# Optimization experiments

Measured on AMD Instinct MI355X. Metric: run time of the kernel, lower is better.

## Reference

```python
import jax, jax.numpy as jnp
import numpy as np

VOCAB = 100000
EMBED = 64
SENT = 20
MEM = 50
BATCH = 32
HOPS = 3
PAD_ID = 0


def position_encoding(sentence_size, embedding_size):
    # Section 4.1 of MemN2N paper, vectorized. Returns [sentence_size, embedding_size].
    i = np.arange(1, embedding_size + 1, dtype=np.float32)[:, None]   # [E,1]
    j = np.arange(1, sentence_size + 1, dtype=np.float32)[None, :]    # [1,S]
    enc = (i - (embedding_size + 1) / 2.0) * (j - (sentence_size + 1) / 2.0)
    enc = 1.0 + 4.0 * enc / embedding_size / sentence_size
    enc[:, -1] = 1.0
    return jnp.asarray(enc.T, dtype=jnp.float32)  # [S,E]


def setup_inputs() -> dict:
    key = jax.random.key(0)
    k1, k2, k3, k4 = jax.random.split(key, 4)
    stories = jax.random.randint(k1, (BATCH, MEM, SENT), 0, VOCAB, dtype=jnp.int64 if jax.config.jax_enable_x64 else jnp.int32)
    queries = jax.random.randint(k2, (BATCH, SENT), 0, VOCAB, dtype=jnp.int64 if jax.config.jax_enable_x64 else jnp.int32)
    A = jax.random.normal(k3, (VOCAB, EMBED), dtype=jnp.float32) * 0.1
    C = jax.random.normal(k4, (HOPS, VOCAB, EMBED), dtype=jnp.float32) * 0.1
    # padding_idx=PAD_ID rows are zero, as in nn.Embedding(padding_idx=...)
    A = A.at[PAD_ID].set(0.0)
    C = C.at[:, PAD_ID].set(0.0)
    encoding = position_encoding(SENT, EMBED)
    return {"stories": stories, "queries": queries, "A": A, "C": C, "encoding": encoding}


def reference(stories, queries, A, C, encoding):
    # queries: [B,S], stories: [B,M,S], A: [V,E], C: [hops,V,E], encoding: [S,E]
    q_emb = A[queries]                                # [B,S,E]
    u = (q_emb * encoding).sum(axis=1)                # [B,E]
    for hop in range(HOPS):
        table_in = A if hop == 0 else C[hop - 1]
        emb_A = table_in[stories]                     # [B,M,S,E]
        m = (emb_A * encoding).sum(axis=2)            # [B,M,E]
        dotted = jnp.einsum('bme,be->bm', m, u)       # [B,M]
        probs = jax.nn.softmax(dotted, axis=-1)       # [B,M]
        emb_C = C[hop][stories]                       # [B,M,S,E]
        c = (emb_C * encoding).sum(axis=2)            # [B,M,E]
        o = jnp.einsum('bm,bme->be', probs, c)        # [B,E]
        u = u + o
    return u @ C[-1].T                                # [B,V]
```

## Files before the change

kernel.cpp:

```cpp
#include <hip/hip_runtime.h>
#include <hip/hip_bf16.h>

#define VOCAB 100000
#define EMBED 64
#define SENT  20
#define MEM   50
#define BATCH 32
#define HOPS  3

#define NSET  4
#define NSLOT (NSET * BATCH * MEM)
#define NVT   (VOCAB / 16)

typedef __attribute__((ext_vector_type(8))) short short8v;
typedef __attribute__((ext_vector_type(4))) float f32x4;

__device__ __forceinline__ float bfr(unsigned short x) {
    union { unsigned int u; float f; } cv;
    cv.u = ((unsigned int)x) << 16;
    return cv.f;
}

__device__ __forceinline__ bool is_bf16(const void* enc) {
    return ((const unsigned int*)enc)[639] == 0x3F803F80u;
}

template<bool BF>
__device__ __forceinline__ float ldT(const void* p, size_t idx) {
    if constexpr (BF) return bfr(((const unsigned short*)p)[idx]);
    else              return ((const float*)p)[idx];
}

__device__ __forceinline__ float wave_sum(float d) {
#pragma unroll
    for (int off = 32; off > 0; off >>= 1) d += __shfl_xor(d, off, 64);
    return d;
}

template<bool BF>
__device__ __forceinline__ void gather_body(const int* __restrict__ stories,
                                            const int* __restrict__ queries,
                                            const void* __restrict__ A,
                                            const void* __restrict__ C,
                                            const void* __restrict__ enc,
                                            float* __restrict__ mc_ws,
                                            float* __restrict__ u0g)
{
    const int tid = threadIdx.x;
    const int e   = tid & 63;
    const int gw  = blockIdx.x * 4 + (tid >> 6);
    const size_t VE = (size_t)VOCAB * EMBED;

    float encr[SENT];
#pragma unroll
    for (int s = 0; s < SENT; ++s) encr[s] = ldT<BF>(enc, s * EMBED + e);

    if (gw < NSLOT) {
        const int t  = gw / (BATCH * MEM);
        const int bm = gw % (BATCH * MEM);
        const void* T   = (t == 0) ? A : C;
        const size_t to = (t == 0) ? 0 : (size_t)(t - 1) * VE;

        int wst = (e < SENT) ? stories[bm * SENT + e] : 0;
        float acc = 0.f;
#pragma unroll
        for (int s = 0; s < SENT; ++s) {
            int w = __shfl(wst, s, 64);
            acc += ldT<BF>(T, to + (size_t)w * EMBED + e) * encr[s];
        }
        mc_ws[gw * EMBED + e] = acc;
    } else if (gw < NSLOT + BATCH) {
        const int b = gw - NSLOT;
        int wq = (e < SENT) ? queries[b * SENT + e] : 0;
        float u = 0.f;
#pragma unroll
        for (int s = 0; s < SENT; ++s) {
            int w = __shfl(wq, s, 64);
            u += ldT<BF>(A, (size_t)w * EMBED + e) * encr[s];
        }
        u0g[b * EMBED + e] = u;
    }
}

__global__ __launch_bounds__(256) void k_gather(
    const int* __restrict__ stories,
    const int* __restrict__ queries,
    const void* __restrict__ A,
    const void* __restrict__ C,
    const void* __restrict__ enc,
    float* __restrict__ mc_ws,
    float* __restrict__ u0g)
{
    if (is_bf16(enc)) gather_body<true >(stories, queries, A, C, enc, mc_ws, u0g);
    else              gather_body<false>(stories, queries, A, C, enc, mc_ws, u0g);
}

__global__ __launch_bounds__(256) void k_recur2(
    const float* __restrict__ mc_ws,
    const float* __restrict__ u0g,
    float* __restrict__ u3g,
    unsigned short* __restrict__ u3bf)
{
    const int b    = blockIdx.x;
    const int tid  = threadIdx.x;
    const int lane = tid & 63;
    const int widx = tid >> 6;

    __shared__ float mc[NSET][MEM][65];
    __shared__ float uls[EMBED];
    __shared__ float ols[4][EMBED];

    for (int idx = tid; idx < NSET * MEM * 16; idx += 256) {
        int t  = idx / (MEM * 16);
        int r  = idx % (MEM * 16);
        int mm = r >> 4;
        int e4 = r & 15;
        const float4 v = *(const float4*)(mc_ws +
            (((size_t)t * BATCH * MEM) + (size_t)b * MEM + mm) * EMBED + e4 * 4);
        mc[t][mm][e4 * 4 + 0] = v.x;
        mc[t][mm][e4 * 4 + 1] = v.y;
        mc[t][mm][e4 * 4 + 2] = v.z;
        mc[t][mm][e4 * 4 + 3] = v.w;
    }
    if (tid < EMBED) uls[tid] = u0g[b * EMBED + tid];
    __syncthreads();

    for (int hop = 0; hop < HOPS; ++hop) {
        float d = 0.f;
        if (lane < MEM) {
#pragma unroll
            for (int e = 0; e < EMBED; ++e)
                d += mc[hop][lane][e] * uls[e];
        }
        float x = (lane < MEM) ? d : -3.4e38f;
        float mx = x;
#pragma unroll
        for (int off = 32; off > 0; off >>= 1) mx = fmaxf(mx, __shfl_xor(mx, off, 64));
        float ex = (lane < MEM) ? __expf(x - mx) : 0.f;
        float sm = wave_sum(ex);
        float p = ex / sm;

        float o = 0.f;
#pragma unroll
        for (int k = 0; k < 13; ++k) {
            int mm = widx * 13 + k;
            if (mm < MEM)
                o += __shfl(p, mm, 64) * mc[hop + 1][mm][lane];
        }
        ols[widx][lane] = o;
        __syncthreads();
        if (tid < EMBED)
            uls[tid] += ols[0][tid] + ols[1][tid] + ols[2][tid] + ols[3][tid];
        __syncthreads();
    }

    if (tid < EMBED) {
        float uv = uls[tid];
        u3g[b * EMBED + tid] = uv;
        __hip_bfloat16 h = __float2bfloat16(uv);
        u3bf[b * EMBED + tid] = *(unsigned short*)&h;
    }
}

__device__ __forceinline__ void out_f32(const float* __restrict__ u,
                                        const void* __restrict__ Cbase,
                                        void* __restrict__ out)
{
    if (blockIdx.x * 256 >= VOCAB) return;
    __shared__ __align__(16) float su[BATCH * EMBED];
    for (int i = threadIdx.x; i < BATCH * EMBED; i += 256) su[i] = u[i];
    __syncthreads();
    const int v = blockIdx.x * 256 + threadIdx.x;
    if (v >= VOCAB) return;

    const size_t c2_off = (size_t)2 * VOCAB * EMBED;
    float row[EMBED];
    const float4* rp = (const float4*)((const float*)Cbase + c2_off + (size_t)v * EMBED);
#pragma unroll
    for (int i = 0; i < 16; ++i) {
        float4 r = rp[i];
        row[i*4 + 0] = r.x; row[i*4 + 1] = r.y;
        row[i*4 + 2] = r.z; row[i*4 + 3] = r.w;
    }

    float* of = (float*)out;
#pragma unroll
    for (int bb = 0; bb < BATCH; ++bb) {
        const float4* sp = (const float4*)(su + bb * EMBED);
        float acc = 0.f;
#pragma unroll
        for (int e4 = 0; e4 < 16; ++e4) {
            float4 us = sp[e4];
            acc += row[e4*4+0]*us.x + row[e4*4+1]*us.y
                 + row[e4*4+2]*us.z + row[e4*4+3]*us.w;
        }
        of[(size_t)bb * VOCAB + v] = acc;
    }
}

__device__ __forceinline__ void out_mfma(const unsigned short* __restrict__ ubf,
                                         const void* __restrict__ Cbase,
                                         void* __restrict__ out)
{
    const int tid  = threadIdx.x;
    const int tv   = blockIdx.x * 4 + (tid >> 6);
    if (tv >= NVT) return;
    const int lane = tid & 63;
    const int l15  = lane & 15;
    const int lh   = lane >> 4;

    const unsigned short* c2 =
        (const unsigned short*)Cbase + (size_t)2 * VOCAB * EMBED;

    const short8v a00 = *(const short8v*)(ubf + ( 0 + l15) * EMBED +  0 + lh * 8);
    const short8v a01 = *(const short8v*)(ubf + ( 0 + l15) * EMBED + 32 + lh * 8);
    const short8v a10 = *(const short8v*)(ubf + (16 + l15) * EMBED +  0 + lh * 8);
    const short8v a11 = *(const short8v*)(ubf + (16 + l15) * EMBED + 32 + lh * 8);

    const unsigned short* brow = c2 + ((size_t)tv * 16 + l15) * EMBED + lh * 8;
    const short8v b0 = *(const short8v*)(brow);
    const short8v b1 = *(const short8v*)(brow + 32);

    f32x4 acc0 = {0.f, 0.f, 0.f, 0.f};
    f32x4 acc1 = {0.f, 0.f, 0.f, 0.f};
    acc0 = __builtin_amdgcn_mfma_f32_16x16x32_bf16(a00, b0, acc0, 0, 0, 0);
    acc0 = __builtin_amdgcn_mfma_f32_16x16x32_bf16(a01, b1, acc0, 0, 0, 0);
    acc1 = __builtin_amdgcn_mfma_f32_16x16x32_bf16(a10, b0, acc1, 0, 0, 0);
    acc1 = __builtin_amdgcn_mfma_f32_16x16x32_bf16(a11, b1, acc1, 0, 0, 0);

    unsigned short* ob = (unsigned short*)out;
    const int v = tv * 16 + l15;
#pragma unroll
    for (int j = 0; j < 4; ++j) {
        const int br = lh * 4 + j;
        __hip_bfloat16 h0 = __float2bfloat16(acc0[j]);
        ob[(size_t)br * VOCAB + v] = *(unsigned short*)&h0;
        __hip_bfloat16 h1 = __float2bfloat16(acc1[j]);
        ob[(size_t)(16 + br) * VOCAB + v] = *(unsigned short*)&h1;
    }
}

__global__ __launch_bounds__(256) void k_out(const float* __restrict__ u,
                                             const unsigned short* __restrict__ ubf,
                                             const void* __restrict__ Cbase,
                                             const void* __restrict__ enc,
                                             void* __restrict__ out)
{
    if (is_bf16(enc)) out_mfma(ubf, Cbase, out);
    else              out_f32(u, Cbase, out);
}

extern "C" void kernel_launch(void* const* d_in, const int* in_sizes, int n_in,
                              void* d_out, int out_size, void* d_ws, size_t ws_size,
                              hipStream_t stream)
{
    const int*  stories = (const int*)d_in[0];
    const int*  queries = (const int*)d_in[1];
    const void* A       = d_in[2];
    const void* C       = d_in[3];
    const void* enc     = d_in[4];

    float* mc_ws = (float*)d_ws;
    float* u0g   = mc_ws + NSLOT * EMBED;
    float* u3g   = u0g + BATCH * EMBED;
    unsigned short* u3bf = (unsigned short*)(u3g + BATCH * EMBED);

    const int nwaves  = NSLOT + BATCH;
    const int nblocks = (nwaves + 3) / 4;

    const int noutblk = (NVT + 3) / 4;

    k_gather<<<nblocks, 256, 0, stream>>>(stories, queries, A, C, enc, mc_ws, u0g);
    k_recur2<<<BATCH, 256, 0, stream>>>(mc_ws, u0g, u3g, u3bf);
    k_out<<<noutblk, 256, 0, stream>>>(u3g, u3bf, C, enc, d_out);
}
```

Measured before the change: 158.6 us.

## Fuse gather and recurrence via per-batch atomic completion counters

Merges the gather kernel and the per-batch hop recurrence into one kernel. Each wave bumps an atomic counter for its batch, and the last wave to finish runs the three-hop recurrence, reading mc rows straight from global memory instead of staging them in LDS. This removes one kernel launch and lets the recurrence overlap with gathers still running for other batches. In exchange it adds a memset launch, atomic traffic and uncached global reads in the recurrence. Correctness of the mc_ws reads depends on acq_rel ordering across the agent.

```diff
diff --git a/kernel.cpp b/kernel.cpp
--- a/kernel.cpp
+++ b/kernel.cpp
@@ -11,6 +11,7 @@
 #define NSET  4
 #define NSLOT (NSET * BATCH * MEM)
 #define NVT   (VOCAB / 16)
+#define PERB  (NSET * MEM + 1)
 
 typedef __attribute__((ext_vector_type(8))) short short8v;
 typedef __attribute__((ext_vector_type(4))) float f32x4;
@@ -37,14 +38,71 @@
     return d;
 }
 
+__device__ void recur_one(const float* __restrict__ mc_ws,
+                          const float* __restrict__ u0g,
+                          float* __restrict__ u3g,
+                          unsigned short* __restrict__ u3bf,
+                          float* __restrict__ uls,
+                          float* __restrict__ ols,
+                          int b)
+{
+    const int tid  = threadIdx.x;
+    const int lane = tid & 63;
+    const int widx = tid >> 6;
+
+    if (tid < EMBED) uls[tid] = u0g[b * EMBED + tid];
+    __syncthreads();
+
+    for (int hop = 0; hop < HOPS; ++hop) {
+        float d = 0.f;
+        if (lane < MEM) {
+            const float* row = mc_ws +
+                ((size_t)hop * BATCH * MEM + (size_t)b * MEM + lane) * EMBED;
+#pragma unroll
+            for (int e2 = 0; e2 < EMBED; ++e2) d += row[e2] * uls[e2];
+        }
+        float x  = (lane < MEM) ? d : -3.4e38f;
+        float mx = x;
+#pragma unroll
+        for (int off = 32; off > 0; off >>= 1) mx = fmaxf(mx, __shfl_xor(mx, off, 64));
+        float ex = (lane < MEM) ? __expf(x - mx) : 0.f;
+        float sm = wave_sum(ex);
+        float p  = ex / sm;
+
+        float o = 0.f;
+        const float* crow = mc_ws +
+            ((size_t)(hop + 1) * BATCH * MEM + (size_t)b * MEM) * EMBED;
+#pragma unroll
+        for (int k = 0; k < 13; ++k) {
+            int mm = widx * 13 + k;
+            if (mm < MEM)
+                o += __shfl(p, mm, 64) * crow[mm * EMBED + lane];
+        }
+        ols[widx * EMBED + lane] = o;
+        __syncthreads();
+        if (tid < EMBED)
+            uls[tid] += ols[0*EMBED+tid] + ols[1*EMBED+tid]
+                      + ols[2*EMBED+tid] + ols[3*EMBED+tid];
+        __syncthreads();
+    }
+
+    if (tid < EMBED) {
+        float uv = uls[tid];
+        u3g[b * EMBED + tid] = uv;
+        __hip_bfloat16 h = __float2bfloat16(uv);
+        u3bf[b * EMBED + tid] = *(unsigned short*)&h;
+    }
+    __syncthreads();
+}
+
 template<bool BF>
-__device__ __forceinline__ void gather_body(const int* __restrict__ stories,
-                                            const int* __restrict__ queries,
-                                            const void* __restrict__ A,
-                                            const void* __restrict__ C,
-                                            const void* __restrict__ enc,
-                                            float* __restrict__ mc_ws,
-                                            float* __restrict__ u0g)
+__device__ __forceinline__ int gather_body(const int* __restrict__ stories,
+                                           const int* __restrict__ queries,
+                                           const void* __restrict__ A,
+                                           const void* __restrict__ C,
+                                           const void* __restrict__ enc,
+                                           float* __restrict__ mc_ws,
+                                           float* __restrict__ u0g)
 {
     const int tid = threadIdx.x;
     const int e   = tid & 63;
@@ -69,7 +127,8 @@
             acc += ldT<BF>(T, to + (size_t)w * EMBED + e) * encr[s];
         }
         mc_ws[gw * EMBED + e] = acc;
-    } else if (gw < NSLOT + BATCH) {
+        return bm / MEM;
+    } else {
         const int b = gw - NSLOT;
         int wq = (e < SENT) ? queries[b * SENT + e] : 0;
         float u = 0.f;
@@ -79,86 +138,46 @@
             u += ldT<BF>(A, (size_t)w * EMBED + e) * encr[s];
         }
         u0g[b * EMBED + e] = u;
-    }
-}
-
-__global__ __launch_bounds__(256) void k_gather(
+        return b;
+    }
+}
+
+__global__ __launch_bounds__(256) void k_gather_recur(
     const int* __restrict__ stories,
     const int* __restrict__ queries,
     const void* __restrict__ A,
     const void* __restrict__ C,
     const void* __restrict__ enc,
     float* __restrict__ mc_ws,
-    float* __restrict__ u0g)
-{
-    if (is_bf16(enc)) gather_body<true >(stories, queries, A, C, enc, mc_ws, u0g);
-    else              gather_body<false>(stories, queries, A, C, enc, mc_ws, u0g);
-}
-
-__global__ __launch_bounds__(256) void k_recur2(
-    const float* __restrict__ mc_ws,
-    const float* __restrict__ u0g,
+    float* __restrict__ u0g,
     float* __restrict__ u3g,
-    unsigned short* __restrict__ u3bf)
-{
-    const int b    = blockIdx.x;
+    unsigned short* __restrict__ u3bf,
+    unsigned* __restrict__ cnt)
+{
+    __shared__ float uls[EMBED];
+    __shared__ float ols[4 * EMBED];
+    __shared__ int   finishb[4];
+
     const int tid  = threadIdx.x;
     const int lane = tid & 63;
     const int widx = tid >> 6;
 
-    __shared__ float mc[NSET][MEM][65];
-    __shared__ float uls[EMBED];
-    __shared__ float ols[4][EMBED];
-
-    for (int idx = tid; idx < NSET * MEM * 16; idx += 256) {
-        int t  = idx / (MEM * 16);
-        int r  = idx % (MEM * 16);
-        int mm = r >> 4;
-        int e4 = r & 15;
-        const float4 v = *(const float4*)(mc_ws +
-            (((size_t)t * BATCH * MEM) + (size_t)b * MEM + mm) * EMBED + e4 * 4);
-        mc[t][mm][e4 * 4 + 0] = v.x;
-        mc[t][mm][e4 * 4 + 1] = v.y;
-        mc[t][mm][e4 * 4 + 2] = v.z;
-        mc[t][mm][e4 * 4 + 3] = v.w;
-    }
-    if (tid < EMBED) uls[tid] = u0g[b * EMBED + tid];
-    __syncthreads();
-
-    for (int hop = 0; hop < HOPS; ++hop) {
-        float d = 0.f;
-        if (lane < MEM) {
-#pragma unroll
-            for (int e = 0; e < EMBED; ++e)
-                d += mc[hop][lane][e] * uls[e];
-        }
-        float x = (lane < MEM) ? d : -3.4e38f;
-        float mx = x;
-#pragma unroll
-        for (int off = 32; off > 0; off >>= 1) mx = fmaxf(mx, __shfl_xor(mx, off, 64));
-        float ex = (lane < MEM) ? __expf(x - mx) : 0.f;
-        float sm = wave_sum(ex);
-        float p = ex / sm;
-
-        float o = 0.f;
-#pragma unroll
-        for (int k = 0; k < 13; ++k) {
-            int mm = widx * 13 + k;
-            if (mm < MEM)
-                o += __shfl(p, mm, 64) * mc[hop + 1][mm][lane];
-        }
-        ols[widx][lane] = o;
-        __syncthreads();
-        if (tid < EMBED)
-            uls[tid] += ols[0][tid] + ols[1][tid] + ols[2][tid] + ols[3][tid];
-        __syncthreads();
-    }
-
-    if (tid < EMBED) {
-        float uv = uls[tid];
-        u3g[b * EMBED + tid] = uv;
-        __hip_bfloat16 h = __float2bfloat16(uv);
-        u3bf[b * EMBED + tid] = *(unsigned short*)&h;
+    int b;
+    if (is_bf16(enc)) b = gather_body<true >(stories, queries, A, C, enc, mc_ws, u0g);
+    else              b = gather_body<false>(stories, queries, A, C, enc, mc_ws, u0g);
+
+    if (lane == 0) {
+        unsigned old = __hip_atomic_fetch_add(&cnt[b], 1u, __ATOMIC_ACQ_REL,
+                                              __HIP_MEMORY_SCOPE_AGENT);
+        finishb[widx] = (old == (unsigned)(PERB - 1)) ? b : -1;
+    }
+    __syncthreads();
+
+#pragma unroll
+    for (int w = 0; w < 4; ++w) {
+        const int fb = finishb[w];
+        if (fb >= 0)
+            recur_one(mc_ws, u0g, u3g, u3bf, uls, ols, fb);
     }
 }
 
@@ -264,13 +283,14 @@
     float* u0g   = mc_ws + NSLOT * EMBED;
     float* u3g   = u0g + BATCH * EMBED;
     unsigned short* u3bf = (unsigned short*)(u3g + BATCH * EMBED);
-
-    const int nwaves  = NSLOT + BATCH;
-    const int nblocks = (nwaves + 3) / 4;
-
+    unsigned* cnt = (unsigned*)(u3bf + BATCH * EMBED);
+
+    const int nblocks = (NSLOT + BATCH) / 4;
     const int noutblk = (NVT + 3) / 4;
 
-    k_gather<<<nblocks, 256, 0, stream>>>(stories, queries, A, C, enc, mc_ws, u0g);
-    k_recur2<<<BATCH, 256, 0, stream>>>(mc_ws, u0g, u3g, u3bf);
+    hipMemsetAsync(cnt, 0, BATCH * sizeof(unsigned), stream);
+
+    k_gather_recur<<<nblocks, 256, 0, stream>>>(stories, queries, A, C, enc,
+                                                mc_ws, u0g, u3g, u3bf, cnt);
     k_out<<<noutblk, 256, 0, stream>>>(u3g, u3bf, C, enc, d_out);
 }
```

New measurement: 330.9 us. 109% more time.
